# Performance work log

Hardware: AMD Instinct MI355X
Metric: run time of the kernel (lower is better)

## Reference

```python
import jax, jax.numpy as jnp
import numpy as np

D = 512
H = 8
DH = D // H
FF = 2 * D
EPS = 1e-5


def _layernorm(x, g, b):
    mu = jnp.mean(x, axis=-1, keepdims=True)
    var = jnp.mean(jnp.square(x - mu), axis=-1, keepdims=True)
    return (x - mu) * jax.lax.rsqrt(var + EPS) * g + b


def setup_inputs() -> dict:
    key = jax.random.key(0)
    ks = jax.random.split(key, 8)
    s = 0.02
    x = jax.random.normal(ks[0], (1, 4096, D), dtype=jnp.float32)
    w_qkv = jax.random.normal(ks[1], (D, 3 * D), dtype=jnp.float32) * s
    b_qkv = jnp.zeros((3 * D,), jnp.float32)
    w_out = jax.random.normal(ks[2], (D, D), dtype=jnp.float32) * s
    b_out = jnp.zeros((D,), jnp.float32)
    w_ff1 = jax.random.normal(ks[3], (D, FF), dtype=jnp.float32) * s
    b_ff1 = jnp.zeros((FF,), jnp.float32)
    w_ff2 = jax.random.normal(ks[4], (FF, D), dtype=jnp.float32) * s
    b_ff2 = jnp.zeros((D,), jnp.float32)
    g1 = jnp.ones((D,), jnp.float32)
    bt1 = jnp.zeros((D,), jnp.float32)
    g2 = jnp.ones((D,), jnp.float32)
    bt2 = jnp.zeros((D,), jnp.float32)
    return {"x": x, "w_qkv": w_qkv, "b_qkv": b_qkv, "w_out": w_out, "b_out": b_out,
            "w_ff1": w_ff1, "b_ff1": b_ff1, "w_ff2": w_ff2, "b_ff2": b_ff2,
            "g1": g1, "bt1": bt1, "g2": g2, "bt2": bt2}


def reference(x, w_qkv, b_qkv, w_out, b_out, w_ff1, b_ff1, w_ff2, b_ff2, g1, bt1, g2, bt2):
    B, S, _ = x.shape
    h = _layernorm(x, g1, bt1)
    qkv = h @ w_qkv + b_qkv                      # [B,S,3D]
    qkv = qkv.reshape(B, S, 3, H, DH)
    q, k, v = qkv[:, :, 0], qkv[:, :, 1], qkv[:, :, 2]   # [B,S,H,DH]
    scores = jnp.einsum('bqhd,bkhd->bhqk', q, k) / np.sqrt(DH).astype(np.float32)
    causal = jnp.tril(jnp.ones((S, S), dtype=bool))
    scores = jnp.where(causal, scores, -jnp.inf)
    attn = jax.nn.softmax(scores, axis=-1)
    out = jnp.einsum('bhqk,bkhd->bqhd', attn, v).reshape(B, S, D)
    x = x + out @ w_out + b_out
    h2 = _layernorm(x, g2, bt2)
    ff = jax.nn.gelu(h2 @ w_ff1 + b_ff1, approximate=False) @ w_ff2 + b_ff2
    return x + ff
```

## Files before the change

### kernel.cpp

```cpp
#include <hip/hip_runtime.h>
#include <math.h>

#define D 512
#define H 8
#define DH 64
#define S 4096
#define FF 1024

typedef __attribute__((ext_vector_type(8))) short bf16x8;
typedef __attribute__((ext_vector_type(4))) float f32x4;
typedef __attribute__((ext_vector_type(16))) float f32x16;

__device__ __forceinline__ unsigned short f2bf(float f) {
    union { float f; unsigned u; } c; c.f = f;
    unsigned r = (c.u + 0x7fff + ((c.u >> 16) & 1)) >> 16;
    return (unsigned short)r;
}
__device__ __forceinline__ float bf2f(unsigned short u) {
    union { unsigned u; float f; } c; c.u = ((unsigned)u) << 16;
    return c.f;
}
__device__ __forceinline__ unsigned asu(float f) {
    union { float f; unsigned u; } c; c.f = f; return c.u;
}

__device__ __forceinline__ void gl_lds16(const void* g, void* l) {
    __builtin_amdgcn_global_load_lds(
        (const __attribute__((address_space(1))) void*)g,
        (__attribute__((address_space(3))) void*)l, 16, 0, 0);
}

__global__ __launch_bounds__(256) void transpose_all(const float* __restrict__ wqkv,
                                                     const float* __restrict__ wout,
                                                     const float* __restrict__ wff1,
                                                     const float* __restrict__ wff2,
                                                     unsigned short* __restrict__ oqkv,
                                                     unsigned short* __restrict__ oout,
                                                     unsigned short* __restrict__ off1,
                                                     unsigned short* __restrict__ off2) {
    __shared__ unsigned short tile[32][33];
    int id = blockIdx.x;
    const float* src; unsigned short* dst; int K, N, lid;
    if (id < 768)       { src = wqkv; dst = oqkv; K = 512;  N = 1536; lid = id; }
    else if (id < 1024) { src = wout; dst = oout; K = 512;  N = 512;  lid = id - 768; }
    else if (id < 1536) { src = wff1; dst = off1; K = 512;  N = 1024; lid = id - 1024; }
    else                { src = wff2; dst = off2; K = 1024; N = 512;  lid = id - 1536; }
    int nb = N / 32;
    int n0 = (lid % nb) * 32, k0 = (lid / nb) * 32;
    int tx = threadIdx.x & 31, ty = threadIdx.x >> 5;
#pragma unroll
    for (int i = 0; i < 32; i += 8)
        tile[ty + i][tx] = f2bf(src[(size_t)(k0 + ty + i) * N + n0 + tx]);
    __syncthreads();
#pragma unroll
    for (int i = 0; i < 32; i += 8)
        dst[(size_t)(n0 + ty + i) * K + k0 + tx] = tile[tx][ty + i];
}

__global__ __launch_bounds__(256) void transpose_v(const unsigned short* __restrict__ qkv,
                                                   unsigned short* __restrict__ vT) {
    __shared__ unsigned short tile[32][33];
    int s0 = blockIdx.x * 32, d0 = blockIdx.y * 32;
    int tx = threadIdx.x & 31, ty = threadIdx.x >> 5;
#pragma unroll
    for (int i = 0; i < 32; i += 8)
        tile[ty + i][tx] = qkv[(size_t)(s0 + ty + i) * (3 * D) + 2 * D + d0 + tx];
    __syncthreads();
#pragma unroll
    for (int i = 0; i < 32; i += 8)
        vT[(size_t)(d0 + ty + i) * S + s0 + tx] = tile[tx][ty + i];
}

__global__ __launch_bounds__(256) void ln_kernel(const float* __restrict__ x,
                                                 const float* __restrict__ g,
                                                 const float* __restrict__ bta,
                                                 unsigned short* __restrict__ out) {
    int row = blockIdx.x, tid = threadIdx.x;
    const float* xr = x + (size_t)row * D;
    float2 v = *(const float2*)(xr + tid * 2);
    float s = v.x + v.y;
    float sq = v.x * v.x + v.y * v.y;
#pragma unroll
    for (int m = 1; m < 64; m <<= 1) { s += __shfl_xor(s, m); sq += __shfl_xor(sq, m); }
    __shared__ float red[8];
    int wave = tid >> 6, lane = tid & 63;
    if (lane == 0) { red[wave] = s; red[4 + wave] = sq; }
    __syncthreads();
    s = red[0] + red[1] + red[2] + red[3];
    sq = red[4] + red[5] + red[6] + red[7];
    float mu = s * (1.f / D);
    float var = sq * (1.f / D) - mu * mu;
    float rstd = rsqrtf(var + 1e-5f);
    int i = tid * 2;
    float2 gg = *(const float2*)(g + i);
    float2 bb = *(const float2*)(bta + i);
    out[(size_t)row * D + i]     = f2bf((v.x - mu) * rstd * gg.x + bb.x);
    out[(size_t)row * D + i + 1] = f2bf((v.y - mu) * rstd * gg.y + bb.y);
}

enum { EPI_BF16 = 0, EPI_RESID_F32 = 1, EPI_GELU_BF16 = 2 };

template <int EPI, int WMI>
__global__ __launch_bounds__(256, WMI == 4 ? 3 : 4)
void gemm2_kernel(const unsigned short* __restrict__ A,
                  const unsigned short* __restrict__ BT,
                  const float* __restrict__ bias,
                  const float* __restrict__ resid,
                  void* __restrict__ out,
                  int M, int N, int K) {
    constexpr int BM = 32 * WMI;
    constexpr int BN = 128;
    constexpr int APH = BM * 8 / 256;
    __shared__ __align__(16) unsigned short sA[BM * 64];
    __shared__ __align__(16) unsigned short sB[BN * 64];

    int tid = threadIdx.x;
    int wave = tid >> 6, lane = tid & 63;
    int quad = lane >> 4, l16 = lane & 15;
    int lx = l16 & 7;
    int wr = (wave >> 1) * (BM / 2), wc = (wave & 1) * 64;
    int m0 = blockIdx.y * BM, n0 = blockIdx.x * BN;

    f32x4 acc[WMI][4];
#pragma unroll
    for (int i = 0; i < WMI; i++)
#pragma unroll
        for (int j = 0; j < 4; j++) acc[i][j] = (f32x4){0.f, 0.f, 0.f, 0.f};

    int srow = tid >> 3;
    int spc = tid & 7;
    int scc = spc ^ (srow & 7);
    const unsigned short* Abase = A + (size_t)(m0 + srow) * K + scc * 8;
    const unsigned short* Bbase = BT + (size_t)(n0 + srow) * K + scc * 8;
    unsigned short* sAdst = sA + (tid & ~63) * 8;
    unsigned short* sBdst = sB + (tid & ~63) * 8;

    for (int k0 = 0; k0 < K; k0 += 64) {
        __syncthreads();
#pragma unroll
        for (int ph = 0; ph < APH; ph++)
            gl_lds16(Abase + (size_t)(ph * 32) * K + k0, sAdst + ph * 256 * 8);
#pragma unroll
        for (int ph = 0; ph < 4; ph++)
            gl_lds16(Bbase + (size_t)(ph * 32) * K + k0, sBdst + ph * 256 * 8);
        asm volatile("s_waitcnt vmcnt(0)" ::: "memory");
        __syncthreads();

#pragma unroll
        for (int ks = 0; ks < 2; ks++) {
            int cxs = ((ks * 4 + quad) ^ lx) * 8;
            bf16x8 af[WMI], bfr[4];
#pragma unroll
            for (int mi = 0; mi < WMI; mi++)
                af[mi] = *(const bf16x8*)(sA + (wr + mi * 16 + l16) * 64 + cxs);
#pragma unroll
            for (int ni = 0; ni < 4; ni++)
                bfr[ni] = *(const bf16x8*)(sB + (wc + ni * 16 + l16) * 64 + cxs);
#pragma unroll
            for (int mi = 0; mi < WMI; mi++)
#pragma unroll
                for (int ni = 0; ni < 4; ni++)
                    acc[mi][ni] = __builtin_amdgcn_mfma_f32_16x16x32_bf16(af[mi], bfr[ni], acc[mi][ni], 0, 0, 0);
        }
    }

#pragma unroll
    for (int mi = 0; mi < WMI; mi++)
#pragma unroll
        for (int ni = 0; ni < 4; ni++) {
            int col = n0 + wc + ni * 16 + l16;
            float bs = bias[col];
#pragma unroll
            for (int r = 0; r < 4; r++) {
                int row = m0 + wr + mi * 16 + quad * 4 + r;
                float v = acc[mi][ni][r] + bs;
                size_t idx = (size_t)row * N + col;
                if constexpr (EPI == EPI_RESID_F32) {
                    ((float*)out)[idx] = v + resid[idx];
                } else if constexpr (EPI == EPI_GELU_BF16) {
                    v = 0.5f * v * (1.f + erff(v * 0.70710678118f));
                    ((unsigned short*)out)[idx] = f2bf(v);
                } else {
                    ((unsigned short*)out)[idx] = f2bf(v);
                }
            }
        }
}

#define LDF 72
#define LDO 68

__global__ __launch_bounds__(256, 4) void flash6_kernel(const unsigned short* __restrict__ qkv,
                                                        const unsigned short* __restrict__ vT,
                                                        unsigned short* __restrict__ O_part,
                                                        float* __restrict__ l_part) {
    __shared__ __align__(16) unsigned short sK[2][64 * LDF];
    __shared__ __align__(16) unsigned short sV[2][64 * LDF];

    int tid = threadIdx.x;
    int w = tid >> 6, lane = tid & 63;
    int lq = lane & 31, hb = lane >> 5;

    int h = blockIdx.x & 7;
    int u = blockIdx.x >> 3;
    int Q = 31, c = 0, acc = 0;
    for (int qq = 31; qq >= 0; --qq) {
        int n = (qq >> 2) + 1;
        if (u < acc + n) { Q = qq; c = u - acc; break; }
        acc += n;
    }
    int T = 2 * Q + 2;
    int t0c = c * 8;
    int t1c = min(t0c + 8, T);
    int q0w = Q * 128 + w * 32;
    int qrow = q0w + lq;
    int qmax = q0w + 31;

    const float CEXP = 0.18033688f;

    bf16x8 qf[4];
#pragma unroll
    for (int dc = 0; dc < 4; dc++) {
        bf16x8 qraw = *(const bf16x8*)(qkv + (size_t)qrow * (3 * D) + h * DH + dc * 16 + hb * 8);
        bf16x8 qs;
#pragma unroll
        for (int j = 0; j < 8; j++)
            qs[j] = (short)f2bf(bf2f((unsigned short)qraw[j]) * CEXP);
        qf[dc] = qs;
    }

    f32x16 oa[2];
#pragma unroll
    for (int i = 0; i < 16; i++) { oa[0][i] = 0.f; oa[1][i] = 0.f; }
    float l4[4] = {0.f, 0.f, 0.f, 0.f};

    int rr = tid >> 3;
    int cc8 = (tid & 7) * 8;
    const unsigned short* kgb = qkv + (size_t)rr * (3 * D) + D + h * DH + cc8;
    const unsigned short* vgb = vT + (size_t)(h * DH + rr) * S + cc8;

    bf16x8 gk0, gk1, gv0, gv1;
    auto glb = [&](int t) {
        const unsigned short* kg = kgb + (size_t)t * 64 * (3 * D);
        gk0 = *(const bf16x8*)(kg);
        gk1 = *(const bf16x8*)(kg + (size_t)32 * (3 * D));
        const unsigned short* vg = vgb + t * 64;
        gv0 = *(const bf16x8*)(vg);
        gv1 = *(const bf16x8*)(vg + (size_t)32 * S);
    };

    glb(t0c);
    for (int t = t0c; t < t1c; ++t) {
        int buf = (t - t0c) & 1;
        unsigned short* dk = &sK[buf][rr * LDF + cc8];
        *(bf16x8*)dk = gk0;
        *(bf16x8*)(dk + 32 * LDF) = gk1;
        unsigned short* dv = &sV[buf][rr * LDF + cc8];
        *(bf16x8*)dv = gv0;
        *(bf16x8*)(dv + 32 * LDF) = gv1;
        if (t + 1 < t1c) glb(t + 1);
        __syncthreads();

        if (64 * t > qmax) continue;

        f32x16 sa[2];
#pragma unroll
        for (int i = 0; i < 16; i++) { sa[0][i] = 0.f; sa[1][i] = 0.f; }
#pragma unroll
        for (int kt = 0; kt < 2; kt++)
#pragma unroll
            for (int dc = 0; dc < 4; dc++) {
                bf16x8 kf = *(const bf16x8*)(&sK[buf][(kt * 32 + lq) * LDF + dc * 16 + hb * 8]);
                sa[kt] = __builtin_amdgcn_mfma_f32_32x32x16_bf16(kf, qf[dc], sa[kt], 0, 0, 0);
            }

        bool dmask = (64 * t + 63 > qmax);
        unsigned p2[2][8];
        if (!dmask) {
#pragma unroll
            for (int kt = 0; kt < 2; kt++) {
                float e[16];
#pragma unroll
                for (int r = 0; r < 16; r++) {
                    e[r] = __builtin_amdgcn_exp2f(sa[kt][r]);
                    l4[r & 3] += e[r];
                }
#pragma unroll
                for (int p = 0; p < 8; p++)
                    p2[kt][p] = __builtin_amdgcn_perm(asu(e[2 * p + 1]) + 0x8000u,
                                                      asu(e[2 * p]) + 0x8000u, 0x07060302u);
            }
        } else {
#pragma unroll
            for (int kt = 0; kt < 2; kt++) {
                float e[16];
#pragma unroll
                for (int r = 0; r < 16; r++) {
                    float v = __builtin_amdgcn_exp2f(sa[kt][r]);
                    int key = 64 * t + kt * 32 + (r & 3) + 8 * (r >> 2) + 4 * hb;
                    if (key > qrow) v = 0.f;
                    e[r] = v;
                    l4[r & 3] += v;
                }
#pragma unroll
                for (int p = 0; p < 8; p++)
                    p2[kt][p] = __builtin_amdgcn_perm(asu(e[2 * p + 1]) + 0x8000u,
                                                      asu(e[2 * p]) + 0x8000u, 0x07060302u);
            }
        }

#pragma unroll
        for (int kc = 0; kc < 4; kc++) {
            int kt = kc >> 1;
            int b0i = (kc & 1) * 4;
            unsigned a0 = p2[kt][b0i + 0], a1 = p2[kt][b0i + 1];
            unsigned b0 = p2[kt][b0i + 2], b1 = p2[kt][b0i + 3];
            unsigned s0 = hb ? a0 : b0, s1 = hb ? a1 : b1;
            unsigned x0 = __shfl_xor(s0, 32), x1 = __shfl_xor(s1, 32);
            unsigned l0 = hb ? b0 : a0, l1 = hb ? b1 : a1;
            union { unsigned u[4]; bf16x8 v; } fr;
            fr.u[0] = hb ? x0 : l0;
            fr.u[1] = hb ? x1 : l1;
            fr.u[2] = hb ? l0 : x0;
            fr.u[3] = hb ? l1 : x1;
#pragma unroll
            for (int dt = 0; dt < 2; dt++) {
                bf16x8 vf = *(const bf16x8*)(&sV[buf][(dt * 32 + lq) * LDF + kc * 16 + hb * 8]);
                oa[dt] = __builtin_amdgcn_mfma_f32_32x32x16_bf16(vf, fr.v, oa[dt], 0, 0, 0);
            }
        }
    }

    float lsum = (l4[0] + l4[1]) + (l4[2] + l4[3]);
    lsum += __shfl_xor(lsum, 32);
    if (hb == 0)
        l_part[((size_t)c * H + h) * S + q0w + lq] = lsum;

    __syncthreads();
    unsigned short* sOw = (unsigned short*)sK + w * 32 * LDO;
#pragma unroll
    for (int kt = 0; kt < 2; kt++)
#pragma unroll
        for (int r = 0; r < 16; r++) {
            int d = kt * 32 + (r & 3) + 8 * (r >> 2) + 4 * hb;
            sOw[lq * LDO + d] = f2bf(oa[kt][r]);
        }
    asm volatile("s_waitcnt lgkmcnt(0)" ::: "memory");
    unsigned short* Op = O_part + ((size_t)c * S + q0w) * D + h * DH;
#pragma unroll
    for (int it = 0; it < 4; it++) {
        int rq = (lane >> 3) + it * 8;
        bf16x8 val = *(const bf16x8*)(sOw + rq * LDO + (lane & 7) * 8);
        *(bf16x8*)(Op + (size_t)rq * D + (lane & 7) * 8) = val;
    }
}

__global__ __launch_bounds__(256) void norm_kernel(const unsigned short* __restrict__ O_part,
                                                   const float* __restrict__ l_part,
                                                   unsigned short* __restrict__ O) {
    int idx = blockIdx.x * 256 + threadIdx.x;
    int row = idx >> 9, col = idx & 511;
    int h = col >> 6;
    int nch = ((row >> 7) >> 2) + 1;
    float o = 0.f, l = 0.f;
    for (int cc = 0; cc < nch; cc++) {
        o += bf2f(O_part[((size_t)cc * S + row) * D + col]);
        l += l_part[((size_t)cc * H + h) * S + row];
    }
    O[idx] = f2bf(o / l);
}

extern "C" void kernel_launch(void* const* d_in, const int* in_sizes, int n_in,
                              void* d_out, int out_size, void* d_ws, size_t ws_size,
                              hipStream_t stream) {
    const float* x     = (const float*)d_in[0];
    const float* w_qkv = (const float*)d_in[1];
    const float* b_qkv = (const float*)d_in[2];
    const float* w_out = (const float*)d_in[3];
    const float* b_out = (const float*)d_in[4];
    const float* w_ff1 = (const float*)d_in[5];
    const float* b_ff1 = (const float*)d_in[6];
    const float* w_ff2 = (const float*)d_in[7];
    const float* b_ff2 = (const float*)d_in[8];
    const float* g1    = (const float*)d_in[9];
    const float* bt1   = (const float*)d_in[10];
    const float* g2    = (const float*)d_in[11];
    const float* bt2   = (const float*)d_in[12];

    char* ws = (char*)d_ws;
    size_t off = 0;
    auto alloc = [&](size_t bytes) {
        void* p = ws + off;
        off += (bytes + 255) & ~(size_t)255;
        return p;
    };
    unsigned short* hbuf   = (unsigned short*)alloc((size_t)S * D * 2);
    unsigned short* qkvbuf = (unsigned short*)alloc((size_t)S * 3 * D * 2);
    unsigned short* vTbuf  = (unsigned short*)alloc((size_t)D * S * 2);
    unsigned short* Obuf   = (unsigned short*)alloc((size_t)S * D * 2);
    unsigned short* wqkvT  = (unsigned short*)alloc((size_t)3 * D * D * 2);
    unsigned short* woutT  = (unsigned short*)alloc((size_t)D * D * 2);
    unsigned short* wff1T  = (unsigned short*)alloc((size_t)FF * D * 2);
    unsigned short* wff2T  = (unsigned short*)alloc((size_t)D * FF * 2);
    unsigned short* Opart  = (unsigned short*)alloc((size_t)8 * S * D * 2);
    float*          lpart  = (float*)alloc((size_t)8 * H * S * 4);
    unsigned short* h2buf  = hbuf;
    unsigned short* ff1buf = qkvbuf;
    float*          x2buf  = (float*)Opart;

    transpose_all<<<dim3(2048), 256, 0, stream>>>(w_qkv, w_out, w_ff1, w_ff2,
                                                  wqkvT, woutT, wff1T, wff2T);

    ln_kernel<<<S, 256, 0, stream>>>(x, g1, bt1, hbuf);
    gemm2_kernel<EPI_BF16, 2><<<dim3(12, 64), 256, 0, stream>>>(
        hbuf, wqkvT, b_qkv, nullptr, qkvbuf, S, 3 * D, D);
    transpose_v<<<dim3(S / 32, D / 32), 256, 0, stream>>>(qkvbuf, vTbuf);
    flash6_kernel<<<dim3(1152), 256, 0, stream>>>(qkvbuf, vTbuf, Opart, lpart);
    norm_kernel<<<dim3(S * D / 256), 256, 0, stream>>>(Opart, lpart, Obuf);
    gemm2_kernel<EPI_RESID_F32, 2><<<dim3(4, 64), 256, 0, stream>>>(
        Obuf, woutT, b_out, x, x2buf, S, D, D);
    ln_kernel<<<S, 256, 0, stream>>>(x2buf, g2, bt2, h2buf);
    gemm2_kernel<EPI_GELU_BF16, 2><<<dim3(8, 64), 256, 0, stream>>>(
        h2buf, wff1T, b_ff1, nullptr, ff1buf, S, FF, D);
    gemm2_kernel<EPI_RESID_F32, 2><<<dim3(4, 64), 256, 0, stream>>>(
        ff1buf, wff2T, b_ff2, x2buf, (float*)d_out, S, D, FF);
}
```

Baseline: 205.2 us.

## Stage flash K/V via direct global-to-LDS loads with XOR swizzle, vectorize norm

The attention kernel now stages K and V tiles with global_load_lds straight into an XOR-swizzled unpadded LDS layout instead of going through registers into padded LDS. It also moves the softmax scale from pre-scaled Q onto the scores before exp2, and uses round-to-nearest bf16 packing. The normalization kernel processes eight columns per thread with vector loads and stores. The QKV and FF1 GEMMs switch to a larger tile template parameter with half the grid rows. These changes target register staging cost, bank conflicts and launch or memory granularity, but add a full vmcnt wait per tile and extra multiplies in the softmax.

New measurement: 200.6 us. 1.02x faster.

```diff
diff --git a/kernel.cpp b/kernel.cpp
--- a/kernel.cpp
+++ b/kernel.cpp
@@ -19,9 +19,6 @@
 __device__ __forceinline__ float bf2f(unsigned short u) {
     union { unsigned u; float f; } c; c.u = ((unsigned)u) << 16;
     return c.f;
-}
-__device__ __forceinline__ unsigned asu(float f) {
-    union { float f; unsigned u; } c; c.f = f; return c.u;
 }
 
 __device__ __forceinline__ void gl_lds16(const void* g, void* l) {
@@ -187,15 +184,13 @@
         }
 }
 
-#define LDF 72
 #define LDO 68
 
-__global__ __launch_bounds__(256, 4) void flash6_kernel(const unsigned short* __restrict__ qkv,
+__global__ __launch_bounds__(256, 4) void flash8_kernel(const unsigned short* __restrict__ qkv,
                                                         const unsigned short* __restrict__ vT,
                                                         unsigned short* __restrict__ O_part,
                                                         float* __restrict__ l_part) {
-    __shared__ __align__(16) unsigned short sK[2][64 * LDF];
-    __shared__ __align__(16) unsigned short sV[2][64 * LDF];
+    __shared__ __align__(16) unsigned short sMem[4][64 * 64];
 
     int tid = threadIdx.x;
     int w = tid >> 6, lane = tid & 63;
@@ -220,14 +215,8 @@
 
     bf16x8 qf[4];
 #pragma unroll
-    for (int dc = 0; dc < 4; dc++) {
-        bf16x8 qraw = *(const bf16x8*)(qkv + (size_t)qrow * (3 * D) + h * DH + dc * 16 + hb * 8);
-        bf16x8 qs;
-#pragma unroll
-        for (int j = 0; j < 8; j++)
-            qs[j] = (short)f2bf(bf2f((unsigned short)qraw[j]) * CEXP);
-        qf[dc] = qs;
-    }
+    for (int dc = 0; dc < 4; dc++)
+        qf[dc] = *(const bf16x8*)(qkv + (size_t)qrow * (3 * D) + h * DH + dc * 16 + hb * 8);
 
     f32x16 oa[2];
 #pragma unroll
@@ -235,31 +224,28 @@
     float l4[4] = {0.f, 0.f, 0.f, 0.f};
 
     int rr = tid >> 3;
-    int cc8 = (tid & 7) * 8;
-    const unsigned short* kgb = qkv + (size_t)rr * (3 * D) + D + h * DH + cc8;
-    const unsigned short* vgb = vT + (size_t)(h * DH + rr) * S + cc8;
-
-    bf16x8 gk0, gk1, gv0, gv1;
-    auto glb = [&](int t) {
+    int spc = tid & 7;
+    int scc = spc ^ (rr & 7);
+    const unsigned short* kgb = qkv + (size_t)rr * (3 * D) + D + h * DH + scc * 8;
+    const unsigned short* vgb = vT + (size_t)(h * DH + rr) * S + scc * 8;
+
+    auto stage = [&](int t, int buf) {
         const unsigned short* kg = kgb + (size_t)t * 64 * (3 * D);
-        gk0 = *(const bf16x8*)(kg);
-        gk1 = *(const bf16x8*)(kg + (size_t)32 * (3 * D));
         const unsigned short* vg = vgb + t * 64;
-        gv0 = *(const bf16x8*)(vg);
-        gv1 = *(const bf16x8*)(vg + (size_t)32 * S);
+        unsigned short* dK = sMem[buf] + w * 512;
+        unsigned short* dV = sMem[2 + buf] + w * 512;
+        gl_lds16(kg, dK);
+        gl_lds16(kg + (size_t)32 * (3 * D), dK + 2048);
+        gl_lds16(vg, dV);
+        gl_lds16(vg + (size_t)32 * S, dV + 2048);
     };
 
-    glb(t0c);
+    stage(t0c, 0);
     for (int t = t0c; t < t1c; ++t) {
         int buf = (t - t0c) & 1;
-        unsigned short* dk = &sK[buf][rr * LDF + cc8];
-        *(bf16x8*)dk = gk0;
-        *(bf16x8*)(dk + 32 * LDF) = gk1;
-        unsigned short* dv = &sV[buf][rr * LDF + cc8];
-        *(bf16x8*)dv = gv0;
-        *(bf16x8*)(dv + 32 * LDF) = gv1;
-        if (t + 1 < t1c) glb(t + 1);
+        asm volatile("s_waitcnt vmcnt(0)" ::: "memory");
         __syncthreads();
+        if (t + 1 < t1c) stage(t + 1, buf ^ 1);
 
         if (64 * t > qmax) continue;
 
@@ -270,8 +256,9 @@
         for (int kt = 0; kt < 2; kt++)
 #pragma unroll
             for (int dc = 0; dc < 4; dc++) {
-                bf16x8 kf = *(const bf16x8*)(&sK[buf][(kt * 32 + lq) * LDF + dc * 16 + hb * 8]);
-                sa[kt] = __builtin_amdgcn_mfma_f32_32x32x16_bf16(kf, qf[dc], sa[kt], 0, 0, 0);
+                int ch = ((dc * 2 + hb) ^ (lq & 7)) * 8;
+                bf16x8 kfr = *(const bf16x8*)(&sMem[buf][(kt * 32 + lq) * 64 + ch]);
+                sa[kt] = __builtin_amdgcn_mfma_f32_32x32x16_bf16(kfr, qf[dc], sa[kt], 0, 0, 0);
             }
 
         bool dmask = (64 * t + 63 > qmax);
@@ -282,13 +269,12 @@
                 float e[16];
 #pragma unroll
                 for (int r = 0; r < 16; r++) {
-                    e[r] = __builtin_amdgcn_exp2f(sa[kt][r]);
+                    e[r] = __builtin_amdgcn_exp2f(sa[kt][r] * CEXP);
                     l4[r & 3] += e[r];
                 }
 #pragma unroll
                 for (int p = 0; p < 8; p++)
-                    p2[kt][p] = __builtin_amdgcn_perm(asu(e[2 * p + 1]) + 0x8000u,
-                                                      asu(e[2 * p]) + 0x8000u, 0x07060302u);
+                    p2[kt][p] = ((unsigned)f2bf(e[2 * p + 1]) << 16) | f2bf(e[2 * p]);
             }
         } else {
 #pragma unroll
@@ -296,7 +282,7 @@
                 float e[16];
 #pragma unroll
                 for (int r = 0; r < 16; r++) {
-                    float v = __builtin_amdgcn_exp2f(sa[kt][r]);
+                    float v = __builtin_amdgcn_exp2f(sa[kt][r] * CEXP);
                     int key = 64 * t + kt * 32 + (r & 3) + 8 * (r >> 2) + 4 * hb;
                     if (key > qrow) v = 0.f;
                     e[r] = v;
@@ -304,8 +290,7 @@
                 }
 #pragma unroll
                 for (int p = 0; p < 8; p++)
-                    p2[kt][p] = __builtin_amdgcn_perm(asu(e[2 * p + 1]) + 0x8000u,
-                                                      asu(e[2 * p]) + 0x8000u, 0x07060302u);
+                    p2[kt][p] = ((unsigned)f2bf(e[2 * p + 1]) << 16) | f2bf(e[2 * p]);
             }
         }
 
@@ -325,8 +310,9 @@
             fr.u[3] = hb ? l1 : x1;
 #pragma unroll
             for (int dt = 0; dt < 2; dt++) {
-                bf16x8 vf = *(const bf16x8*)(&sV[buf][(dt * 32 + lq) * LDF + kc * 16 + hb * 8]);
-                oa[dt] = __builtin_amdgcn_mfma_f32_32x32x16_bf16(vf, fr.v, oa[dt], 0, 0, 0);
+                int ch = ((kc * 2 + hb) ^ (lq & 7)) * 8;
+                bf16x8 vfr = *(const bf16x8*)(&sMem[2 + buf][(dt * 32 + lq) * 64 + ch]);
+                oa[dt] = __builtin_amdgcn_mfma_f32_32x32x16_bf16(vfr, fr.v, oa[dt], 0, 0, 0);
             }
         }
     }
@@ -337,7 +323,7 @@
         l_part[((size_t)c * H + h) * S + q0w + lq] = lsum;
 
     __syncthreads();
-    unsigned short* sOw = (unsigned short*)sK + w * 32 * LDO;
+    unsigned short* sOw = (unsigned short*)sMem + w * 32 * LDO;
 #pragma unroll
     for (int kt = 0; kt < 2; kt++)
 #pragma unroll
@@ -359,15 +345,23 @@
                                                    const float* __restrict__ l_part,
                                                    unsigned short* __restrict__ O) {
     int idx = blockIdx.x * 256 + threadIdx.x;
-    int row = idx >> 9, col = idx & 511;
-    int h = col >> 6;
+    int row = idx >> 6;
+    int c8 = (idx & 63) * 8;
+    int h = c8 >> 6;
     int nch = ((row >> 7) >> 2) + 1;
-    float o = 0.f, l = 0.f;
+    float o[8] = {0.f, 0.f, 0.f, 0.f, 0.f, 0.f, 0.f, 0.f};
+    float l = 0.f;
     for (int cc = 0; cc < nch; cc++) {
-        o += bf2f(O_part[((size_t)cc * S + row) * D + col]);
+        bf16x8 v = *(const bf16x8*)(O_part + ((size_t)cc * S + row) * D + c8);
+#pragma unroll
+        for (int j = 0; j < 8; j++) o[j] += bf2f((unsigned short)v[j]);
         l += l_part[((size_t)cc * H + h) * S + row];
     }
-    O[idx] = f2bf(o / l);
+    float inv = 1.f / l;
+    bf16x8 r;
+#pragma unroll
+    for (int j = 0; j < 8; j++) r[j] = (short)f2bf(o[j] * inv);
+    *(bf16x8*)(O + (size_t)row * D + c8) = r;
 }
 
 extern "C" void kernel_launch(void* const* d_in, const int* in_sizes, int n_in,
@@ -412,15 +406,15 @@
                                                   wqkvT, woutT, wff1T, wff2T);
 
     ln_kernel<<<S, 256, 0, stream>>>(x, g1, bt1, hbuf);
-    gemm2_kernel<EPI_BF16, 2><<<dim3(12, 64), 256, 0, stream>>>(
+    gemm2_kernel<EPI_BF16, 4><<<dim3(12, 32), 256, 0, stream>>>(
         hbuf, wqkvT, b_qkv, nullptr, qkvbuf, S, 3 * D, D);
     transpose_v<<<dim3(S / 32, D / 32), 256, 0, stream>>>(qkvbuf, vTbuf);
-    flash6_kernel<<<dim3(1152), 256, 0, stream>>>(qkvbuf, vTbuf, Opart, lpart);
-    norm_kernel<<<dim3(S * D / 256), 256, 0, stream>>>(Opart, lpart, Obuf);
+    flash8_kernel<<<dim3(1152), 256, 0, stream>>>(qkvbuf, vTbuf, Opart, lpart);
+    norm_kernel<<<dim3(S * D / 8 / 256), 256, 0, stream>>>(Opart, lpart, Obuf);
     gemm2_kernel<EPI_RESID_F32, 2><<<dim3(4, 64), 256, 0, stream>>>(
         Obuf, woutT, b_out, x, x2buf, S, D, D);
     ln_kernel<<<S, 256, 0, stream>>>(x2buf, g2, bt2, h2buf);
-    gemm2_kernel<EPI_GELU_BF16, 2><<<dim3(8, 64), 256, 0, stream>>>(
+    gemm2_kernel<EPI_GELU_BF16, 4><<<dim3(8, 32), 256, 0, stream>>>(
         h2buf, wff1T, b_ff1, nullptr, ff1buf, S, FF, D);
     gemm2_kernel<EPI_RESID_F32, 2><<<dim3(4, 64), 256, 0, stream>>>(
         ff1buf, wff2T, b_ff2, x2buf, (float*)d_out, S, D, FF);
```
